# Performance work log

Hardware: AMD Instinct MI355X
Metric: run time of the kernel (lower is better)

## Reference

```python
import jax, jax.numpy as jnp
import numpy as np

D_M, L_OBS, ALPHA, D_H = 1024, 2048, 8192, 2048


def setup_inputs() -> dict:
    key = jax.random.key(0)
    k1, k2, k3, k4, k5 = jax.random.split(key, 5)
    x_ts = jax.random.normal(k1, (D_M, L_OBS), dtype=jnp.float32)
    t_ts = jax.random.randint(k2, (D_M, L_OBS), 0, ALPHA, dtype=jnp.int32)
    global_means = jax.random.normal(k3, (D_M,), dtype=jnp.float32)
    W = jax.random.normal(k4, (D_H, D_M), dtype=jnp.float32) * 0.02
    b = jax.random.normal(k5, (D_H,), dtype=jnp.float32) * 0.02
    return {"x_ts": x_ts, "t_ts": t_ts, "global_means": global_means, "W": W, "b": b}


def reference(x_ts, t_ts, global_means, W, b):
    d_m, l_obs = x_ts.shape
    alpha = ALPHA
    # valid observations: non-NaN value and time index within [0, alpha)
    valid = (~jnp.isnan(x_ts)) & (t_ts >= 0) & (t_ts < alpha)
    # route invalid observations to a dummy column `alpha` (dropped afterwards)
    idx = jnp.where(valid, t_ts, alpha)                      # [d_m, l_obs]
    rows = jnp.arange(d_m)[:, None]
    xs = jnp.where(valid, x_ts, 0.0)
    grid_val = jnp.zeros((d_m, alpha + 1), x_ts.dtype).at[rows, idx].set(xs)[:, :alpha]
    grid_ok = jnp.zeros((d_m, alpha + 1), bool).at[rows, idx].set(valid)[:, :alpha]
    # forward-fill: last valid index via cummax, init with global mean
    pos = jnp.arange(alpha)[None, :]                         # [1, alpha]
    last = jax.lax.cummax(jnp.where(grid_ok, pos, -1), axis=1)  # [d_m, alpha]
    filled = jnp.take_along_axis(grid_val, jnp.maximum(last, 0), axis=1)
    regular = jnp.where(last >= 0, filled, global_means[:, None])  # [d_m, alpha]
    # 1x1 conv over time == GEMM over feature dim; output [alpha, d_h]
    return jnp.einsum('ma,hm->ah', regular, W) + b[None, :]
```

## Files before the change

kernel.cpp:

```cpp
#include <hip/hip_runtime.h>
#include <stdint.h>

#define D_M   1024
#define L_OBS 2048
#define ALPHA 8192
#define D_H   2048

typedef __attribute__((ext_vector_type(8))) short short8;
typedef __attribute__((ext_vector_type(4))) float f32x4;

__device__ inline unsigned short f2bf(float f) {
  union { float f; unsigned u; } c; c.f = f;
  unsigned u = c.u;
  u += 0x7fffu + ((u >> 16) & 1u);
  return (unsigned short)(u >> 16);
}

__global__ __launch_bounds__(1024) void impute_fill(
    const float* __restrict__ x_ts, const int* __restrict__ t_ts,
    const float* __restrict__ gmean, unsigned short* __restrict__ dst,
    int transposed_out) {
  __shared__ unsigned long long pack[ALPHA];
  __shared__ float s_wv[16];
  __shared__ int   s_wh[16];

  const int m    = blockIdx.x;
  const int tid  = threadIdx.x;
  const int lane = tid & 63;
  const int wv   = tid >> 6;

  #pragma unroll
  for (int i = 0; i < 8; ++i) pack[tid + i * 1024] = 0ull;
  __syncthreads();

  #pragma unroll
  for (int j = 0; j < 2; ++j) {
    const int l = tid + j * 1024;
    const float xv = x_ts[(size_t)m * L_OBS + l];
    const int   tv = t_ts[(size_t)m * L_OBS + l];
    if ((xv == xv) && (tv >= 0) && (tv < ALPHA)) {
      union { float f; unsigned u; } c; c.f = xv;
      atomicMax(&pack[tv], ((unsigned long long)(l + 1) << 32) | c.u);
    }
  }
  __syncthreads();

  const int base = tid * 8;
  int has = 0; float lv = 0.f;
  #pragma unroll
  for (int i = 0; i < 8; ++i) {
    const unsigned long long p = pack[base + i];
    if (p >> 32) { has = 1; lv = __uint_as_float((unsigned)p); }
  }

  int ihas = has; float ilv = lv;
  #pragma unroll
  for (int d = 1; d < 64; d <<= 1) {
    const float pv = __shfl_up(ilv, d, 64);
    const int   ph = __shfl_up(ihas, d, 64);
    if (lane >= d && !ihas) { ihas = ph; ilv = pv; }
  }
  if (lane == 63) { s_wh[wv] = ihas; s_wv[wv] = ilv; }
  __syncthreads();
  if (wv == 0 && lane < 16) {
    int h2 = s_wh[lane]; float v2 = s_wv[lane];
    #pragma unroll
    for (int d = 1; d < 16; d <<= 1) {
      const float pv = __shfl_up(v2, d, 16);
      const int   ph = __shfl_up(h2, d, 16);
      if (lane >= d && !h2) { h2 = ph; v2 = pv; }
    }
    s_wh[lane] = h2; s_wv[lane] = v2;
  }
  __syncthreads();

  const float xlv = __shfl_up(ilv, 1, 64);
  const int   xh_ = __shfl_up(ihas, 1, 64);
  const int   xhas = (lane > 0) ? xh_ : 0;
  float running;
  if (xhas)                         running = xlv;
  else if (wv > 0 && s_wh[wv - 1])  running = s_wv[wv - 1];
  else                              running = gmean[m];

  if (transposed_out) {
    #pragma unroll
    for (int i = 0; i < 8; ++i) {
      const unsigned long long p = pack[base + i];
      if (p >> 32) running = __uint_as_float((unsigned)p);
      dst[(size_t)(base + i) * D_M + m] = f2bf(running);
    }
  } else {
    short8 ov;
    #pragma unroll
    for (int i = 0; i < 8; ++i) {
      const unsigned long long p = pack[base + i];
      if (p >> 32) running = __uint_as_float((unsigned)p);
      ov[i] = (short)f2bf(running);
    }
    *(short8*)&dst[(size_t)m * ALPHA + base] = ov;
  }
}

__global__ __launch_bounds__(256) void transpose_bf(
    const unsigned short* __restrict__ reg, unsigned short* __restrict__ regT) {
  __shared__ unsigned short tile[64 * 64];
  const int t  = threadIdx.x;
  const int m0 = (blockIdx.x & 15) * 64;
  const int A0 = (blockIdx.x >> 4) * 64;

  #pragma unroll
  for (int i = 0; i < 2; ++i) {
    const int m  = i * 32 + (t >> 3);
    const int ao = (t & 7) * 8;
    short8 v = *(const short8*)&reg[(size_t)(m0 + m) * ALPHA + A0 + ao];
    const int s = ((m & 7) ^ (m >> 3)) << 3;
    *(short8*)&tile[m * 64 + (ao ^ s)] = v;
  }
  __syncthreads();
  #pragma unroll
  for (int i = 0; i < 2; ++i) {
    const int a  = i * 32 + (t >> 3);
    const int mo = (t & 7) * 8;
    short8 ov;
    #pragma unroll
    for (int j = 0; j < 8; ++j) {
      const int mm = mo + j;
      const int s  = ((mm & 7) ^ (mm >> 3)) << 3;
      ov[j] = (short)tile[mm * 64 + (a ^ s)];
    }
    *(short8*)&regT[(size_t)(A0 + a) * D_M + m0 + mo] = ov;
  }
}

__global__ __launch_bounds__(256) void wconv(const float* __restrict__ W,
                                             unsigned short* __restrict__ Wb) {
  const int i = (blockIdx.x * 256 + threadIdx.x) * 4;
  const float4 w = *reinterpret_cast<const float4*>(&W[i]);
  ushort4 o;
  o.x = f2bf(w.x); o.y = f2bf(w.y); o.z = f2bf(w.z); o.w = f2bf(w.w);
  *reinterpret_cast<ushort4*>(&Wb[i]) = o;
}

#define GNT 16

__device__ inline void gload_lds16(const void* g, void* l) {
  __builtin_amdgcn_global_load_lds(
      (const __attribute__((address_space(1))) unsigned int*)g,
      (__attribute__((address_space(3))) unsigned int*)l, 16, 0, 0);
}

#define BARX() { asm volatile("" ::: "memory"); __builtin_amdgcn_s_barrier(); \
                 asm volatile("" ::: "memory"); }

__global__ __launch_bounds__(512, 2) void gemm_bias(
    const unsigned short* __restrict__ A,
    const unsigned short* __restrict__ B,
    const float* __restrict__ bias, float* __restrict__ out) {
  __shared__ char lds[131072];

  const int tid  = threadIdx.x;
  const int lane = tid & 63;
  const int wid  = tid >> 6;
  const int wm   = wid >> 2;
  const int wn   = wid & 3;
  const int bn   = blockIdx.x & 7;
  const int bm   = blockIdx.x >> 3;
  const int a0 = bm * 256, h0 = bn * 256;

  f32x4 acc[8][4] = {};
  short8 af[8], bf[2];

  const int r0 = tid >> 2, s0 = tid & 3;
  const int swzB = (s0 ^ ((r0 >> 1) & 3)) * 16;
  const char* Asrc0 = (const char*)A + ((size_t)(a0 + r0) * D_M) * 2 + swzB;
  const char* Asrc1 = Asrc0 + (size_t)128 * D_M * 2;
  const char* Bsrc0 = (const char*)B + ((size_t)(h0 + r0) * D_M) * 2 + swzB;
  const char* Bsrc1 = Bsrc0 + (size_t)128 * D_M * 2;

#define STAGE_A(kh) { char* d_ = lds + ((kh) & 3) * 16384 + tid * 16; \
  gload_lds16(Asrc0 + (size_t)(kh) * 64, d_); \
  gload_lds16(Asrc1 + (size_t)(kh) * 64, d_ + 8192); }
#define STAGE_B(kh) { char* d_ = lds + 65536 + ((kh) & 3) * 16384 + tid * 16; \
  gload_lds16(Bsrc0 + (size_t)(kh) * 64, d_); \
  gload_lds16(Bsrc1 + (size_t)(kh) * 64, d_ + 8192); }

  const int rl  = lane & 15;
  const int rsw = (((lane >> 4) ^ ((rl >> 1) & 3))) * 16;
  const int Aro = (wm * 128 + rl) * 64 + rsw;
  const int Bro = 65536 + (wn * 64 + rl) * 64 + rsw;

#define RD_A(kh) { _Pragma("unroll") \
  for (int mf = 0; mf < 8; ++mf) \
    af[mf] = *(const short8*)(lds + ((kh) & 3) * 16384 + Aro + mf * 1024); }
#define RD_B(kh, np) { \
  bf[0] = *(const short8*)(lds + ((kh) & 3) * 16384 + Bro + ((np) * 2 + 0) * 1024); \
  bf[1] = *(const short8*)(lds + ((kh) & 3) * 16384 + Bro + ((np) * 2 + 1) * 1024); }

#define PH_MFMA(NP) \
  BARX(); \
  asm volatile("s_waitcnt lgkmcnt(0)" ::: "memory"); \
  __builtin_amdgcn_sched_barrier(0); \
  __builtin_amdgcn_s_setprio(1); \
  _Pragma("unroll") \
  for (int mf = 0; mf < 8; ++mf) { \
    acc[mf][(NP)*2+0] = __builtin_amdgcn_mfma_f32_16x16x32_bf16(af[mf], bf[0], acc[mf][(NP)*2+0], 0, 0, 0); \
    acc[mf][(NP)*2+1] = __builtin_amdgcn_mfma_f32_16x16x32_bf16(af[mf], bf[1], acc[mf][(NP)*2+1], 0, 0, 0); \
  } \
  __builtin_amdgcn_s_setprio(0); \
  BARX();

  STAGE_A(0); STAGE_B(0); STAGE_A(1); STAGE_B(1); STAGE_A(2); STAGE_B(2); STAGE_A(3);
  asm volatile("s_waitcnt vmcnt(6)" ::: "memory");
  BARX();

  for (int t = 0; t < GNT - 2; ++t) {
    const int kh0 = 2 * t, kh1 = 2 * t + 1;
    RD_A(kh0); RD_B(kh0, 0);
    STAGE_B(kh0 + 3);
    PH_MFMA(0);
    RD_B(kh0, 1);
    STAGE_A(kh0 + 4);
    PH_MFMA(1);
    RD_A(kh1); RD_B(kh1, 0);
    STAGE_B(kh0 + 4);
    PH_MFMA(0);
    RD_B(kh1, 1);
    STAGE_A(kh0 + 5);
    asm volatile("s_waitcnt vmcnt(6)" ::: "memory");
    PH_MFMA(1);
  }
  {
    RD_A(28); RD_B(28, 0);
    STAGE_B(31);
    PH_MFMA(0);
    RD_B(28, 1);
    PH_MFMA(1);
    RD_A(29); RD_B(29, 0);
    PH_MFMA(0);
    RD_B(29, 1);
    asm volatile("s_waitcnt vmcnt(4)" ::: "memory");
    PH_MFMA(1);
  }
  {
    RD_A(30); RD_B(30, 0);
    PH_MFMA(0);
    RD_B(30, 1);
    asm volatile("s_waitcnt vmcnt(0)" ::: "memory");
    PH_MFMA(1);
    RD_A(31); RD_B(31, 0);
    PH_MFMA(0);
    RD_B(31, 1);
    PH_MFMA(1);
  }

  const int cl = lane & 15, rq = lane >> 4;
  #pragma unroll
  for (int n = 0; n < 4; ++n) {
    const int h = h0 + wn * 64 + n * 16 + cl;
    const float bv = bias[h];
    #pragma unroll
    for (int f = 0; f < 8; ++f) {
      const int ar = a0 + wm * 128 + f * 16 + rq * 4;
      #pragma unroll
      for (int r = 0; r < 4; ++r)
        out[(size_t)(ar + r) * D_H + h] = acc[f][n][r] + bv;
    }
  }
#undef STAGE_A
#undef STAGE_B
#undef RD_A
#undef RD_B
#undef PH_MFMA
}

extern "C" void kernel_launch(void* const* d_in, const int* in_sizes, int n_in,
                              void* d_out, int out_size, void* d_ws, size_t ws_size,
                              hipStream_t stream) {
  const float* x  = (const float*)d_in[0];
  const int*   t  = (const int*)d_in[1];
  const float* gm = (const float*)d_in[2];
  const float* W  = (const float*)d_in[3];
  const float* b  = (const float*)d_in[4];
  float* out = (float*)d_out;

  const size_t SZ_REG = (size_t)ALPHA * D_M * 2;
  const size_t SZ_WB  = (size_t)D_H * D_M * 2;

  if (ws_size >= 2 * SZ_REG + SZ_WB) {
    unsigned short* reg  = (unsigned short*)d_ws;
    unsigned short* regT = (unsigned short*)((char*)d_ws + SZ_REG);
    unsigned short* Wb   = (unsigned short*)((char*)d_ws + 2 * SZ_REG);
    impute_fill<<<D_M, 1024, 0, stream>>>(x, t, gm, reg, 0);
    wconv<<<(D_H * D_M) / 1024, 256, 0, stream>>>(W, Wb);
    transpose_bf<<<(ALPHA / 64) * (D_M / 64), 256, 0, stream>>>(reg, regT);
    gemm_bias<<<(ALPHA / 256) * (D_H / 256), 512, 0, stream>>>(regT, Wb, b, out);
  } else {
    unsigned short* regT = (unsigned short*)d_ws;
    unsigned short* Wb   = (unsigned short*)((char*)d_ws + SZ_REG);
    impute_fill<<<D_M, 1024, 0, stream>>>(x, t, gm, regT, 1);
    wconv<<<(D_H * D_M) / 1024, 256, 0, stream>>>(W, Wb);
    gemm_bias<<<(ALPHA / 256) * (D_H / 256), 512, 0, stream>>>(regT, Wb, b, out);
  }
}
```

Baseline: 66.42 us.

## Double-buffer GEMM fragment registers to overlap LDS reads with MFMA

The bf16 GEMM main loop now keeps two sets of A/B fragment registers and issues LDS reads for the next phase before running MFMAs on the current phase. This removes the old pattern of a barrier plus a full lgkmcnt wait right before every MFMA block. The loop is manually unrolled over explicit LDS stage indices, with a longer hand-written epilogue. In exchange, register pressure rises because twice as many fragments are live, which could cause spills at the launch bound of 512 threads with 2 blocks per CU.

Result: slower. 68.58 us (+3.3%).

```diff
diff --git a/kernel.cpp b/kernel.cpp
--- a/kernel.cpp
+++ b/kernel.cpp
@@ -151,6 +151,8 @@
 
 #define BARX() { asm volatile("" ::: "memory"); __builtin_amdgcn_s_barrier(); \
                  asm volatile("" ::: "memory"); }
+#define LGKM0() asm volatile("s_waitcnt lgkmcnt(0)" ::: "memory")
+#define SB0()   __builtin_amdgcn_sched_barrier(0)
 
 __global__ __launch_bounds__(512, 2) void gemm_bias(
     const unsigned short* __restrict__ A,
@@ -165,22 +167,22 @@
   const int wn   = wid & 3;
   const int bn   = blockIdx.x & 7;
   const int bm   = blockIdx.x >> 3;
-  const int a0 = bm * 256, h0 = bn * 256;
+  const int a0r = bm * 256, h0 = bn * 256;
 
   f32x4 acc[8][4] = {};
-  short8 af[8], bf[2];
+  short8 a0[8], a1[8], b0[2], b1[2];
 
   const int r0 = tid >> 2, s0 = tid & 3;
   const int swzB = (s0 ^ ((r0 >> 1) & 3)) * 16;
-  const char* Asrc0 = (const char*)A + ((size_t)(a0 + r0) * D_M) * 2 + swzB;
+  const char* Asrc0 = (const char*)A + ((size_t)(a0r + r0) * D_M) * 2 + swzB;
   const char* Asrc1 = Asrc0 + (size_t)128 * D_M * 2;
   const char* Bsrc0 = (const char*)B + ((size_t)(h0 + r0) * D_M) * 2 + swzB;
   const char* Bsrc1 = Bsrc0 + (size_t)128 * D_M * 2;
 
-#define STAGE_A(kh) { char* d_ = lds + ((kh) & 3) * 16384 + tid * 16; \
+#define STAGE_A_S(S, kh) { char* d_ = lds + (S) * 16384 + tid * 16; \
   gload_lds16(Asrc0 + (size_t)(kh) * 64, d_); \
   gload_lds16(Asrc1 + (size_t)(kh) * 64, d_ + 8192); }
-#define STAGE_B(kh) { char* d_ = lds + 65536 + ((kh) & 3) * 16384 + tid * 16; \
+#define STAGE_B_S(S, kh) { char* d_ = lds + 65536 + (S) * 16384 + tid * 16; \
   gload_lds16(Bsrc0 + (size_t)(kh) * 64, d_); \
   gload_lds16(Bsrc1 + (size_t)(kh) * 64, d_ + 8192); }
 
@@ -189,69 +191,109 @@
   const int Aro = (wm * 128 + rl) * 64 + rsw;
   const int Bro = 65536 + (wn * 64 + rl) * 64 + rsw;
 
-#define RD_A(kh) { _Pragma("unroll") \
-  for (int mf = 0; mf < 8; ++mf) \
-    af[mf] = *(const short8*)(lds + ((kh) & 3) * 16384 + Aro + mf * 1024); }
-#define RD_B(kh, np) { \
-  bf[0] = *(const short8*)(lds + ((kh) & 3) * 16384 + Bro + ((np) * 2 + 0) * 1024); \
-  bf[1] = *(const short8*)(lds + ((kh) & 3) * 16384 + Bro + ((np) * 2 + 1) * 1024); }
-
-#define PH_MFMA(NP) \
-  BARX(); \
-  asm volatile("s_waitcnt lgkmcnt(0)" ::: "memory"); \
-  __builtin_amdgcn_sched_barrier(0); \
+#define LDA(S, mf) (*(const short8*)(lds + (S) * 16384 + Aro + (mf) * 1024))
+#define LDB(S, n)  (*(const short8*)(lds + (S) * 16384 + Bro + (n) * 1024))
+
+#define MFMA16(AF, BF, N0, N1) \
   __builtin_amdgcn_s_setprio(1); \
   _Pragma("unroll") \
   for (int mf = 0; mf < 8; ++mf) { \
-    acc[mf][(NP)*2+0] = __builtin_amdgcn_mfma_f32_16x16x32_bf16(af[mf], bf[0], acc[mf][(NP)*2+0], 0, 0, 0); \
-    acc[mf][(NP)*2+1] = __builtin_amdgcn_mfma_f32_16x16x32_bf16(af[mf], bf[1], acc[mf][(NP)*2+1], 0, 0, 0); \
+    acc[mf][N0] = __builtin_amdgcn_mfma_f32_16x16x32_bf16(AF[mf], BF[0], acc[mf][N0], 0, 0, 0); \
+    acc[mf][N1] = __builtin_amdgcn_mfma_f32_16x16x32_bf16(AF[mf], BF[1], acc[mf][N1], 0, 0, 0); \
   } \
-  __builtin_amdgcn_s_setprio(0); \
-  BARX();
-
-  STAGE_A(0); STAGE_B(0); STAGE_A(1); STAGE_B(1); STAGE_A(2); STAGE_B(2); STAGE_A(3);
+  __builtin_amdgcn_s_setprio(0);
+
+#define TILE(S0, S1, S2, S3, KH0) { \
+   \
+  LGKM0(); SB0(); \
+  b1[0] = LDB(S0, 2); b1[1] = LDB(S0, 3); \
+  a1[0] = LDA(S1, 0); a1[1] = LDA(S1, 1); a1[2] = LDA(S1, 2); a1[3] = LDA(S1, 3); \
+  STAGE_B_S(S3, (KH0) + 3); \
+  SB0(); \
+  MFMA16(a0, b0, 0, 1); \
+  asm volatile("s_waitcnt vmcnt(6)" ::: "memory"); \
+  BARX(); \
+   \
+  LGKM0(); SB0(); \
+  a1[4] = LDA(S1, 4); a1[5] = LDA(S1, 5); a1[6] = LDA(S1, 6); a1[7] = LDA(S1, 7); \
+  b0[0] = LDB(S1, 0); b0[1] = LDB(S1, 1); \
+  STAGE_A_S(S0, (KH0) + 4); \
+  SB0(); \
+  MFMA16(a0, b1, 2, 3); \
+  BARX(); \
+   \
+  LGKM0(); SB0(); \
+  b1[0] = LDB(S1, 2); b1[1] = LDB(S1, 3); \
+  a0[0] = LDA(S2, 0); a0[1] = LDA(S2, 1); a0[2] = LDA(S2, 2); a0[3] = LDA(S2, 3); \
+  STAGE_B_S(S0, (KH0) + 4); \
+  SB0(); \
+  MFMA16(a1, b0, 0, 1); \
+  asm volatile("s_waitcnt vmcnt(6)" ::: "memory"); \
+  BARX(); \
+   \
+  LGKM0(); SB0(); \
+  a0[4] = LDA(S2, 4); a0[5] = LDA(S2, 5); a0[6] = LDA(S2, 6); a0[7] = LDA(S2, 7); \
+  b0[0] = LDB(S2, 0); b0[1] = LDB(S2, 1); \
+  STAGE_A_S(S1, (KH0) + 5); \
+  SB0(); \
+  MFMA16(a1, b1, 2, 3); \
+  BARX(); \
+}
+
+  STAGE_A_S(0, 0); STAGE_B_S(0, 0); STAGE_A_S(1, 1); STAGE_B_S(1, 1);
+  STAGE_A_S(2, 2); STAGE_B_S(2, 2); STAGE_A_S(3, 3);
   asm volatile("s_waitcnt vmcnt(6)" ::: "memory");
   BARX();
-
-  for (int t = 0; t < GNT - 2; ++t) {
-    const int kh0 = 2 * t, kh1 = 2 * t + 1;
-    RD_A(kh0); RD_B(kh0, 0);
-    STAGE_B(kh0 + 3);
-    PH_MFMA(0);
-    RD_B(kh0, 1);
-    STAGE_A(kh0 + 4);
-    PH_MFMA(1);
-    RD_A(kh1); RD_B(kh1, 0);
-    STAGE_B(kh0 + 4);
-    PH_MFMA(0);
-    RD_B(kh1, 1);
-    STAGE_A(kh0 + 5);
-    asm volatile("s_waitcnt vmcnt(6)" ::: "memory");
-    PH_MFMA(1);
-  }
-  {
-    RD_A(28); RD_B(28, 0);
-    STAGE_B(31);
-    PH_MFMA(0);
-    RD_B(28, 1);
-    PH_MFMA(1);
-    RD_A(29); RD_B(29, 0);
-    PH_MFMA(0);
-    RD_B(29, 1);
-    asm volatile("s_waitcnt vmcnt(4)" ::: "memory");
-    PH_MFMA(1);
-  }
-  {
-    RD_A(30); RD_B(30, 0);
-    PH_MFMA(0);
-    RD_B(30, 1);
-    asm volatile("s_waitcnt vmcnt(0)" ::: "memory");
-    PH_MFMA(1);
-    RD_A(31); RD_B(31, 0);
-    PH_MFMA(0);
-    RD_B(31, 1);
-    PH_MFMA(1);
-  }
+  a0[0] = LDA(0, 0); a0[1] = LDA(0, 1); a0[2] = LDA(0, 2); a0[3] = LDA(0, 3);
+  a0[4] = LDA(0, 4); a0[5] = LDA(0, 5); a0[6] = LDA(0, 6); a0[7] = LDA(0, 7);
+  b0[0] = LDB(0, 0); b0[1] = LDB(0, 1);
+
+  for (int tt = 0; tt < 7; ++tt) {
+    const int k0 = 4 * tt;
+    TILE(0, 1, 2, 3, k0);
+    TILE(2, 3, 0, 1, k0 + 2);
+  }
+
+  LGKM0(); SB0();
+  b1[0] = LDB(0, 2); b1[1] = LDB(0, 3);
+  a1[0] = LDA(1, 0); a1[1] = LDA(1, 1); a1[2] = LDA(1, 2); a1[3] = LDA(1, 3);
+  STAGE_B_S(3, 31);
+  SB0(); MFMA16(a0, b0, 0, 1);
+  asm volatile("s_waitcnt vmcnt(6)" ::: "memory");
+  BARX();
+  LGKM0(); SB0();
+  a1[4] = LDA(1, 4); a1[5] = LDA(1, 5); a1[6] = LDA(1, 6); a1[7] = LDA(1, 7);
+  b0[0] = LDB(1, 0); b0[1] = LDB(1, 1);
+  SB0(); MFMA16(a0, b1, 2, 3);
+  BARX();
+  LGKM0(); SB0();
+  b1[0] = LDB(1, 2); b1[1] = LDB(1, 3);
+  a0[0] = LDA(2, 0); a0[1] = LDA(2, 1); a0[2] = LDA(2, 2); a0[3] = LDA(2, 3);
+  SB0(); MFMA16(a1, b0, 0, 1);
+  asm volatile("s_waitcnt vmcnt(2)" ::: "memory");
+  BARX();
+  LGKM0(); SB0();
+  a0[4] = LDA(2, 4); a0[5] = LDA(2, 5); a0[6] = LDA(2, 6); a0[7] = LDA(2, 7);
+  b0[0] = LDB(2, 0); b0[1] = LDB(2, 1);
+  SB0(); MFMA16(a1, b1, 2, 3);
+  BARX();
+  LGKM0(); SB0();
+  b1[0] = LDB(2, 2); b1[1] = LDB(2, 3);
+  a1[0] = LDA(3, 0); a1[1] = LDA(3, 1); a1[2] = LDA(3, 2); a1[3] = LDA(3, 3);
+  SB0(); MFMA16(a0, b0, 0, 1);
+  asm volatile("s_waitcnt vmcnt(0)" ::: "memory");
+  BARX();
+  LGKM0(); SB0();
+  a1[4] = LDA(3, 4); a1[5] = LDA(3, 5); a1[6] = LDA(3, 6); a1[7] = LDA(3, 7);
+  b0[0] = LDB(3, 0); b0[1] = LDB(3, 1);
+  SB0(); MFMA16(a0, b1, 2, 3);
+  BARX();
+  LGKM0(); SB0();
+  b1[0] = LDB(3, 2); b1[1] = LDB(3, 3);
+  SB0(); MFMA16(a1, b0, 0, 1);
+  BARX();
+  LGKM0(); SB0();
+  MFMA16(a1, b1, 2, 3);
 
   const int cl = lane & 15, rq = lane >> 4;
   #pragma unroll
@@ -260,17 +302,18 @@
     const float bv = bias[h];
     #pragma unroll
     for (int f = 0; f < 8; ++f) {
-      const int ar = a0 + wm * 128 + f * 16 + rq * 4;
+      const int ar = a0r + wm * 128 + f * 16 + rq * 4;
       #pragma unroll
       for (int r = 0; r < 4; ++r)
         out[(size_t)(ar + r) * D_H + h] = acc[f][n][r] + bv;
     }
   }
-#undef STAGE_A
-#undef STAGE_B
-#undef RD_A
-#undef RD_B
-#undef PH_MFMA
+#undef STAGE_A_S
+#undef STAGE_B_S
+#undef LDA
+#undef LDB
+#undef MFMA16
+#undef TILE
 }
 
 extern "C" void kernel_launch(void* const* d_in, const int* in_sizes, int n_in,
```
